# Kernel tuning notes

Hardware: AMD Instinct MI355X
Metric: run time of the kernel (lower is better)

The kernel has to match this reference:

```python
import jax, jax.numpy as jnp
import numpy as np

B, N, D_IN, D_OUT = 16, 512, 256, 32
C_SP, H, W = 64, 256, 256


def setup_inputs() -> dict:
    key = jax.random.key(0)
    k1, k2, k3, k4, k5 = jax.random.split(key, 5)
    return {
        "spatial_info": jax.random.normal(k1, (B, C_SP, H, W), dtype=jnp.float32),
        "entity_embeddings": jax.random.normal(k2, (B, N, D_IN), dtype=jnp.float32),
        "W_proj": jax.random.normal(k3, (D_IN, D_OUT), dtype=jnp.float32) / np.sqrt(D_IN),
        "b_proj": jax.random.normal(k4, (D_OUT,), dtype=jnp.float32) * 0.01,
        "locations": jax.random.randint(k5, (B, N, 2), 0, 256, dtype=jnp.int32),
    }


def reference(spatial_info, entity_embeddings, W_proj, b_proj, locations):
    # per-entity linear projection (fc_block): [B, N, D_out]
    proj = jnp.einsum('bnd,de->bne', entity_embeddings, W_proj) + b_proj

    Bb, C, Hh, Ww = spatial_info.shape
    # clamp locations like the torch min/max logic
    h = jnp.clip(locations[..., 0], 0, Hh - 1)  # [B, N]
    w = jnp.clip(locations[..., 1], 0, Ww - 1)  # [B, N]
    flat = h * Ww + w                            # [B, N] flattened spatial index

    scatter_map = jnp.zeros((Bb, Hh * Ww, proj.shape[-1]), dtype=spatial_info.dtype)
    b_idx = jnp.arange(Bb, dtype=flat.dtype)[:, None]  # [B, 1]
    scatter_map = scatter_map.at[b_idx, flat].set(proj)
    scatter_map = scatter_map.reshape(Bb, Hh, Ww, -1).transpose(0, 3, 1, 2)  # [B, D_out, H, W]

    return jnp.concatenate([spatial_info, scatter_map], axis=1)
```

## Files before the change

kernel.cpp:

```cpp
#include <hip/hip_runtime.h>

#define BATCH 16
#define NENT  512
#define D_IN  256
#define D_OUT 32
#define CSP   64
#define COUT  96
#define HWDIM 256
#define HWSZ  65536
#define HW4   16384
#define SP_B4  (CSP * HW4)
#define OUT_B4 (COUT * HW4)

__global__ void init_proj_kernel(const float* __restrict__ emb,
                                 const float* __restrict__ Wp,
                                 const float* __restrict__ bp,
                                 int4* __restrict__ owner4,
                                 float* __restrict__ projbuf) {
    int tid = blockIdx.x * blockDim.x + threadIdx.x;
    const int NZ4 = BATCH * HWSZ / 4;
    if (tid < NZ4) {
        owner4[tid] = make_int4(0, 0, 0, 0);
        return;
    }
    int gid = tid - NZ4;
    int ent = gid >> 5;
    int e   = gid & 31;
    float acc = bp[e];
    const float* er = emb + ent * D_IN;
    #pragma unroll 8
    for (int d = 0; d < D_IN; ++d) {
        acc += er[d] * Wp[d * D_OUT + e];
    }
    projbuf[gid] = acc;
}

__global__ void owner_kernel(const int* __restrict__ loc,
                             int* __restrict__ owner) {
    int gid = blockIdx.x * blockDim.x + threadIdx.x;
    if (gid >= BATCH * NENT) return;
    int h = loc[gid * 2 + 0];
    int w = loc[gid * 2 + 1];
    h = min(max(h, 0), HWDIM - 1);
    w = min(max(w, 0), HWDIM - 1);
    int b = gid >> 9;
    int n = gid & (NENT - 1);
    atomicMax(&owner[b * HWSZ + h * HWDIM + w], n + 1);
}

__global__ void fused_out_kernel(const float4* __restrict__ sp,
                                 const int4* __restrict__ owner4,
                                 const float* __restrict__ projbuf,
                                 float4* __restrict__ out) {
    int tid  = blockIdx.x * blockDim.x + threadIdx.x;
    int hw4  = tid & (HW4 - 1);
    int rest = tid >> 14;
    int half = rest & 1;
    int b    = rest >> 1;

    const float4* s = sp + (b * CSP + 32 * half) * HW4 + hw4;
    float4*       o = out + b * OUT_B4 + 32 * half * HW4 + hw4;

    #pragma unroll 8
    for (int c = 0; c < 32; ++c) {
        o[c * HW4] = s[c * HW4];
    }

    int4 ow = owner4[b * HW4 + hw4];
    const float* pb = projbuf + b * (NENT * D_OUT) + 16 * half;
    float4* oz = out + b * OUT_B4 + (CSP + 16 * half) * HW4 + hw4;
    #pragma unroll 4
    for (int e = 0; e < 16; ++e) {
        float4 v;
        v.x = ow.x ? pb[(ow.x - 1) * D_OUT + e] : 0.f;
        v.y = ow.y ? pb[(ow.y - 1) * D_OUT + e] : 0.f;
        v.z = ow.z ? pb[(ow.z - 1) * D_OUT + e] : 0.f;
        v.w = ow.w ? pb[(ow.w - 1) * D_OUT + e] : 0.f;
        oz[e * HW4] = v;
    }
}

extern "C" void kernel_launch(void* const* d_in, const int* in_sizes, int n_in,
                              void* d_out, int out_size, void* d_ws, size_t ws_size,
                              hipStream_t stream) {
    const float* spatial = (const float*)d_in[0];
    const float* emb     = (const float*)d_in[1];
    const float* Wp      = (const float*)d_in[2];
    const float* bp      = (const float*)d_in[3];
    const int*   loc     = (const int*)d_in[4];
    float* out = (float*)d_out;

    int*   owner   = (int*)d_ws;
    float* projbuf = (float*)((char*)d_ws + BATCH * HWSZ * sizeof(int));

    init_proj_kernel<<<2048, 256, 0, stream>>>(emb, Wp, bp, (int4*)owner, projbuf);
    owner_kernel<<<32, 256, 0, stream>>>(loc, owner);
    fused_out_kernel<<<2048, 256, 0, stream>>>((const float4*)spatial,
                                               (const int4*)owner, projbuf,
                                               (float4*)out);
}
```

Before: 161.4 us.

## Flatten output kernel to one float4 per thread across a 2D batch grid

Restructures the fused output kernel so each thread copies two spatial float4s and writes a single scatter-channel float4, using a 2D grid with batch on the y axis. This replaces per-thread strided loops over 32 channels with many more independent threads, aiming to raise memory-level parallelism for a bandwidth-bound copy. The owner map is now re-read once per output channel, which relies on cache hits, and block count grows sixteenfold.

```diff
diff --git a/kernel.cpp b/kernel.cpp
--- a/kernel.cpp
+++ b/kernel.cpp
@@ -10,6 +10,7 @@
 #define HWSZ  65536
 #define HW4   16384
 #define SP_B4  (CSP * HW4)
+#define SC_B4  (D_OUT * HW4)
 #define OUT_B4 (COUT * HW4)
 
 __global__ void init_proj_kernel(const float* __restrict__ emb,
@@ -52,32 +53,26 @@
                                  const int4* __restrict__ owner4,
                                  const float* __restrict__ projbuf,
                                  float4* __restrict__ out) {
-    int tid  = blockIdx.x * blockDim.x + threadIdx.x;
-    int hw4  = tid & (HW4 - 1);
-    int rest = tid >> 14;
-    int half = rest & 1;
-    int b    = rest >> 1;
+    const int PER = 2048 * 256;
+    int b = blockIdx.y;
+    int t = blockIdx.x * blockDim.x + threadIdx.x;
 
-    const float4* s = sp + (b * CSP + 32 * half) * HW4 + hw4;
-    float4*       o = out + b * OUT_B4 + 32 * half * HW4 + hw4;
+    const float4* spb  = sp  + (size_t)b * SP_B4;
+    float4*       outb = out + (size_t)b * OUT_B4;
 
-    #pragma unroll 8
-    for (int c = 0; c < 32; ++c) {
-        o[c * HW4] = s[c * HW4];
-    }
+    outb[t]        = spb[t];
+    outb[t + PER]  = spb[t + PER];
 
+    int e   = t >> 14;
+    int hw4 = t & (HW4 - 1);
     int4 ow = owner4[b * HW4 + hw4];
-    const float* pb = projbuf + b * (NENT * D_OUT) + 16 * half;
-    float4* oz = out + b * OUT_B4 + (CSP + 16 * half) * HW4 + hw4;
-    #pragma unroll 4
-    for (int e = 0; e < 16; ++e) {
-        float4 v;
-        v.x = ow.x ? pb[(ow.x - 1) * D_OUT + e] : 0.f;
-        v.y = ow.y ? pb[(ow.y - 1) * D_OUT + e] : 0.f;
-        v.z = ow.z ? pb[(ow.z - 1) * D_OUT + e] : 0.f;
-        v.w = ow.w ? pb[(ow.w - 1) * D_OUT + e] : 0.f;
-        oz[e * HW4] = v;
-    }
+    const float* pb = projbuf + b * (NENT * D_OUT) + e;
+    float4 v;
+    v.x = ow.x ? pb[(ow.x - 1) * D_OUT] : 0.f;
+    v.y = ow.y ? pb[(ow.y - 1) * D_OUT] : 0.f;
+    v.z = ow.z ? pb[(ow.z - 1) * D_OUT] : 0.f;
+    v.w = ow.w ? pb[(ow.w - 1) * D_OUT] : 0.f;
+    outb[SP_B4 + t] = v;
 }
 
 extern "C" void kernel_launch(void* const* d_in, const int* in_sizes, int n_in,
@@ -95,7 +90,8 @@
 
     init_proj_kernel<<<2048, 256, 0, stream>>>(emb, Wp, bp, (int4*)owner, projbuf);
     owner_kernel<<<32, 256, 0, stream>>>(loc, owner);
-    fused_out_kernel<<<2048, 256, 0, stream>>>((const float4*)spatial,
+    dim3 grid(2048, BATCH);
+    fused_out_kernel<<<grid, 256, 0, stream>>>((const float4*)spatial,
                                                (const int4*)owner, projbuf,
                                                (float4*)out);
 }
```

Result: faster. 143.4 us (-11.2%).
